# Performance work log

Measured on AMD Instinct MI355X. Metric: run time of the kernel, lower is better.

Reference implementation:

```python
import jax, jax.numpy as jnp
import numpy as np

EPS = 1e-5
DECAY = 0.9        # membrane potential decay
SLOPE = 0.01       # leaky_relu negative slope
HEBB_LR = 0.01     # Hebbian plasticity learning rate
WD = 1e-3          # synapse weight decay
W_CLAMP = 1.0      # synapse weight clamp


def _ln(x, g, b):
    mu = jnp.mean(x, axis=-1, keepdims=True)
    var = jnp.mean((x - mu) ** 2, axis=-1, keepdims=True)
    return (x - mu) * jax.lax.rsqrt(var + EPS) * g + b


def setup_inputs() -> dict:
    key = jax.random.key(0)
    ks = jax.random.split(key, 4)
    B, N = 16384, 1024
    scale = 1.0 / np.sqrt(N)
    return {
        "inputs": jax.random.normal(ks[0], (B, N), dtype=jnp.float32),
        "contribution": jax.random.uniform(ks[1], (B,), dtype=jnp.float32),
        "prev_potential": jnp.zeros((B, N), dtype=jnp.float32),
        "syn_weights": jax.random.normal(ks[2], (N, N), dtype=jnp.float32) * scale,
        "gate_W": jax.random.normal(ks[3], (N, N), dtype=jnp.float32) * scale,
        "gate_b": jnp.zeros((N,), dtype=jnp.float32),
        "pre_gamma": jnp.ones((N,), dtype=jnp.float32),
        "pre_beta": jnp.zeros((N,), dtype=jnp.float32),
        "ln_gamma": jnp.ones((N,), dtype=jnp.float32),
        "ln_beta": jnp.zeros((N,), dtype=jnp.float32),
    }


def reference(inputs, contribution, prev_potential, syn_weights, gate_W, gate_b,
              pre_gamma, pre_beta, ln_gamma, ln_beta):
    B = inputs.shape[0]
    # pre-norm
    x_norm = _ln(inputs, pre_gamma, pre_beta)
    # neuron: recurrent drive through synapse weights + leaky membrane
    pre = x_norm @ syn_weights                      # [B, N]
    potential = DECAY * prev_potential + pre        # new neuron state
    activation = jnp.where(potential >= 0, potential, SLOPE * potential)
    # Hebbian synapse update modulated by per-sample contribution
    hebb = jnp.einsum('bi,bj->ij', activation * contribution[:, None], activation) / B
    new_syn_weights = jnp.clip(syn_weights * (1.0 - WD) + HEBB_LR * hebb,
                               -W_CLAMP, W_CLAMP)
    # gated residual (gate computed on raw inputs)
    gate = jax.nn.sigmoid(inputs @ gate_W.T + gate_b)
    residual = gate * activation + (1.0 - gate) * inputs
    # post-norm (dropout is identity in eval/reference)
    output = _ln(residual, ln_gamma, ln_beta)
    return (output, potential, new_syn_weights)
```

## Files before the change

### kernel.cpp

```cpp
#include <hip/hip_runtime.h>
#include <cstdint>
#include <cstddef>

#define EPS 1e-5f
#define DECAY 0.9f
#define SLOPE 0.01f
#define HEBB_LR 0.01f
#define WDK 1e-3f

typedef float f32x4 __attribute__((ext_vector_type(4)));
typedef __bf16 bf16x8 __attribute__((ext_vector_type(8)));
typedef unsigned short u16;
typedef unsigned int u32;

union U128 { uint4 u; bf16x8 b; };
union Pack16 { u16 s[16]; uint4 q[2]; };
union Pack8  { u16 s[8];  uint4 q; };
union Pack4  { u16 s[4];  uint2 q; };

__device__ __forceinline__ u16 f2b(float f) {
  u32 u = __builtin_bit_cast(u32, f);
  u = u + 0x7FFFu + ((u >> 16) & 1u);
  return (u16)(u >> 16);
}
__device__ __forceinline__ float b2f(u16 h) {
  u32 u = ((u32)h) << 16;
  return __builtin_bit_cast(float, u);
}
__device__ __forceinline__ float wred(float x) {
#pragma unroll
  for (int o = 32; o > 0; o >>= 1) x += __shfl_down(x, o, 64);
  return x;
}

__device__ __forceinline__ void gld16(const u16* g, u16* lds) {
  __builtin_amdgcn_global_load_lds(
      (__attribute__((address_space(1))) void*)g,
      (__attribute__((address_space(3))) void*)lds, 16, 0, 0);
}

__global__ __launch_bounds__(256) void prep_rows(
    const float* __restrict__ in, const float* __restrict__ pg,
    const float* __restrict__ pb, u16* __restrict__ xnb,
    u16* __restrict__ inb, int N) {
  const int row = blockIdx.x, t = threadIdx.x;
  const float* rp = in + (size_t)row * N;
  float4 v = reinterpret_cast<const float4*>(rp)[t];
  float s = v.x + v.y + v.z + v.w;
  float s2 = v.x * v.x + v.y * v.y + v.z * v.z + v.w * v.w;
  s = wred(s); s2 = wred(s2);
  __shared__ float rs_[4], rs2_[4];
  if ((t & 63) == 0) { rs_[t >> 6] = s; rs2_[t >> 6] = s2; }
  __syncthreads();
  float S = rs_[0] + rs_[1] + rs_[2] + rs_[3];
  float S2 = rs2_[0] + rs2_[1] + rs2_[2] + rs2_[3];
  float mu = S / N;
  float var = S2 / N - mu * mu;
  float rstd = rsqrtf(var + EPS);
  float4 g = reinterpret_cast<const float4*>(pg)[t];
  float4 b = reinterpret_cast<const float4*>(pb)[t];
  float xv[4] = {v.x, v.y, v.z, v.w};
  float gv[4] = {g.x, g.y, g.z, g.w};
  float bv[4] = {b.x, b.y, b.z, b.w};
  Pack4 px, pi;
#pragma unroll
  for (int j = 0; j < 4; ++j) {
    px.s[j] = f2b((xv[j] - mu) * rstd * gv[j] + bv[j]);
    pi.s[j] = f2b(xv[j]);
  }
  reinterpret_cast<uint2*>(xnb + (size_t)row * N)[t] = px.q;
  reinterpret_cast<uint2*>(inb + (size_t)row * N)[t] = pi.q;
}

__global__ __launch_bounds__(256) void wconv(const float* __restrict__ W,
                                             u16* __restrict__ Wb, int total) {
  int idx = blockIdx.x * 256 + threadIdx.x;
  size_t off = (size_t)idx * 8;
  if (off >= (size_t)total) return;
  float4 a = *reinterpret_cast<const float4*>(W + off);
  float4 b = *reinterpret_cast<const float4*>(W + off + 4);
  Pack8 p;
  p.s[0] = f2b(a.x); p.s[1] = f2b(a.y); p.s[2] = f2b(a.z); p.s[3] = f2b(a.w);
  p.s[4] = f2b(b.x); p.s[5] = f2b(b.y); p.s[6] = f2b(b.z); p.s[7] = f2b(b.w);
  *reinterpret_cast<uint4*>(Wb + off) = p.q;
}

__global__ __launch_bounds__(256) void wconv_T(const float* __restrict__ W,
                                               u16* __restrict__ Wt, int R, int C) {
  __shared__ float tile[64][65];
  int c0 = blockIdx.x * 64, r0 = blockIdx.y * 64;
  int tr = threadIdx.x >> 2, tc = threadIdx.x & 3;
#pragma unroll
  for (int cc = 0; cc < 4; ++cc) {
    float4 v = *reinterpret_cast<const float4*>(W + (size_t)(r0 + tr) * C + c0 + tc * 16 + cc * 4);
    tile[tr][tc * 16 + cc * 4 + 0] = v.x;
    tile[tr][tc * 16 + cc * 4 + 1] = v.y;
    tile[tr][tc * 16 + cc * 4 + 2] = v.z;
    tile[tr][tc * 16 + cc * 4 + 3] = v.w;
  }
  __syncthreads();
  Pack16 p;
#pragma unroll
  for (int j = 0; j < 16; ++j) p.s[j] = f2b(tile[tc * 16 + j][tr]);
  uint4* dst = reinterpret_cast<uint4*>(Wt + (size_t)(c0 + tr) * R + r0 + tc * 16);
  dst[0] = p.q[0]; dst[1] = p.q[1];
}

__global__ __launch_bounds__(256) void transpose_act(
    const float* __restrict__ pot, const float* __restrict__ contrib,
    u16* __restrict__ actT, u16* __restrict__ actcT, int Brows, int N) {
  __shared__ float tile[64][65];
  __shared__ float csh[64];
  int n0 = blockIdx.x * 64, b0 = blockIdx.y * 64;
  int tr = threadIdx.x >> 2, tc = threadIdx.x & 3;
  if (threadIdx.x < 64) csh[threadIdx.x] = contrib[b0 + threadIdx.x];
#pragma unroll
  for (int cc = 0; cc < 4; ++cc) {
    float4 v = *reinterpret_cast<const float4*>(pot + (size_t)(b0 + tr) * N + n0 + tc * 16 + cc * 4);
    float a0 = v.x >= 0.f ? v.x : SLOPE * v.x;
    float a1 = v.y >= 0.f ? v.y : SLOPE * v.y;
    float a2 = v.z >= 0.f ? v.z : SLOPE * v.z;
    float a3 = v.w >= 0.f ? v.w : SLOPE * v.w;
    tile[tr][tc * 16 + cc * 4 + 0] = a0;
    tile[tr][tc * 16 + cc * 4 + 1] = a1;
    tile[tr][tc * 16 + cc * 4 + 2] = a2;
    tile[tr][tc * 16 + cc * 4 + 3] = a3;
  }
  __syncthreads();
  Pack16 pa, pc;
#pragma unroll
  for (int j = 0; j < 16; ++j) {
    float a = tile[tc * 16 + j][tr];
    pa.s[j] = f2b(a);
    pc.s[j] = f2b(a * csh[tc * 16 + j]);
  }
  size_t obase = (size_t)(n0 + tr) * Brows + b0 + tc * 16;
  uint4* d1 = reinterpret_cast<uint4*>(actT + obase);
  d1[0] = pa.q[0]; d1[1] = pa.q[1];
  uint4* d2 = reinterpret_cast<uint4*>(actcT + obase);
  d2[0] = pc.q[0]; d2[1] = pc.q[1];
}

__global__ __launch_bounds__(256) void fuse_out(
    const float* __restrict__ pot, const u16* __restrict__ gate,
    const u16* __restrict__ inb, const float* __restrict__ lg,
    const float* __restrict__ lb, float* __restrict__ out, int N) {
  const int row = blockIdx.x, t = threadIdx.x;
  size_t base = (size_t)row * N;
  float4 p = reinterpret_cast<const float4*>(pot + base)[t];
  Pack4 xq; xq.q = reinterpret_cast<const uint2*>(inb + base)[t];
  Pack4 gq; gq.q = reinterpret_cast<const uint2*>(gate + base)[t];
  float pv[4] = {p.x, p.y, p.z, p.w};
  float res[4];
  float s = 0.f, s2 = 0.f;
#pragma unroll
  for (int j = 0; j < 4; ++j) {
    float a = pv[j] >= 0.f ? pv[j] : SLOPE * pv[j];
    float gv = b2f(gq.s[j]);
    float xv = b2f(xq.s[j]);
    float r = gv * a + (1.f - gv) * xv;
    res[j] = r; s += r; s2 += r * r;
  }
  s = wred(s); s2 = wred(s2);
  __shared__ float rs_[4], rs2_[4];
  if ((t & 63) == 0) { rs_[t >> 6] = s; rs2_[t >> 6] = s2; }
  __syncthreads();
  float S = rs_[0] + rs_[1] + rs_[2] + rs_[3];
  float S2 = rs2_[0] + rs2_[1] + rs2_[2] + rs2_[3];
  float mu = S / N, var = S2 / N - mu * mu, rstd = rsqrtf(var + EPS);
  float4 g4 = reinterpret_cast<const float4*>(lg)[t];
  float4 b4 = reinterpret_cast<const float4*>(lb)[t];
  float gv[4] = {g4.x, g4.y, g4.z, g4.w}, bv[4] = {b4.x, b4.y, b4.z, b4.w};
  float4 o;
  o.x = (res[0] - mu) * rstd * gv[0] + bv[0];
  o.y = (res[1] - mu) * rstd * gv[1] + bv[1];
  o.z = (res[2] - mu) * rstd * gv[2] + bv[2];
  o.w = (res[3] - mu) * rstd * gv[3] + bv[3];
  reinterpret_cast<float4*>(out + base)[t] = o;
}

template <int EPI>
__global__ __launch_bounds__(512, 2) void gemm2p(
    const u16* __restrict__ A, const u16* __restrict__ Bt,
    int lda, int NT, int Ncols,
    const float* __restrict__ aux,
    float* __restrict__ outF, u16* __restrict__ outB,
    int nbx, int nbxShift, int nbyX) {
  __shared__ __align__(128) char lds[131072];
  const int tid = threadIdx.x;
  const int w = tid >> 6, l = tid & 63;
  const int wr = w >> 2, wc = w & 3;
  const int r16 = l & 15, gq = l >> 4;

  int bx, by, kb;
  if (EPI == 2) {
    bx = blockIdx.x; by = blockIdx.y; kb = blockIdx.z * NT * 64;
  } else {
    int bid = blockIdx.x;
    int xcd = bid & 7, i = bid >> 3;
    by = xcd * nbyX + (i >> nbxShift);
    bx = i & (nbx - 1);
    kb = 0;
  }
  const int m0 = by * 256, n0 = bx * 256;

  const u16* gA[4]; const u16* gB[4]; int dOff[4];
#pragma unroll
  for (int i = 0; i < 4; ++i) {
    int c = i * 512 + tid;
    int row = c >> 3;
    int kg = (c & 7) ^ (row & 7);
    gA[i] = A + (size_t)(m0 + row) * (size_t)lda + kb + kg * 8;
    gB[i] = Bt + (size_t)(n0 + row) * (size_t)lda + kb + kg * 8;
    dOff[i] = c * 16;
  }

  int pA[8], pB[4], kgx[2];
#pragma unroll
  for (int mf = 0; mf < 8; ++mf) pA[mf] = (wr * 128 + mf * 16 + r16) * 128;
#pragma unroll
  for (int nf = 0; nf < 4; ++nf) pB[nf] = (wc * 64 + nf * 16 + r16) * 128;
  kgx[0] = ((gq) ^ (r16 & 7)) * 16;
  kgx[1] = ((4 + gq) ^ (r16 & 7)) * 16;

  f32x4 acc[8][4] = {};

#define STAGE_(t, bufb) { const int _kk = (t) * 64;                           \
  _Pragma("unroll") for (int i = 0; i < 4; ++i)                               \
    gld16(gA[i] + _kk, (u16*)(lds + (bufb) + dOff[i]));                       \
  _Pragma("unroll") for (int i = 0; i < 4; ++i)                               \
    gld16(gB[i] + _kk, (u16*)(lds + (bufb) + 32768 + dOff[i])); }

  STAGE_(0, 0);
  __syncthreads();

  int buf = 0;
  for (int t = 0; t < NT; ++t) {
    if (t + 1 < NT) STAGE_(t + 1, (buf ^ 1) * 65536);
    const char* Ab = lds + buf * 65536;
    const char* Bb = Ab + 32768;
#pragma unroll
    for (int ks = 0; ks < 2; ++ks) {
      U128 af[8], bf[4];
#pragma unroll
      for (int mf = 0; mf < 8; ++mf)
        af[mf].u = *reinterpret_cast<const uint4*>(Ab + pA[mf] + kgx[ks]);
#pragma unroll
      for (int nf = 0; nf < 4; ++nf)
        bf[nf].u = *reinterpret_cast<const uint4*>(Bb + pB[nf] + kgx[ks]);
      __builtin_amdgcn_s_setprio(1);
#pragma unroll
      for (int mf = 0; mf < 8; ++mf)
#pragma unroll
        for (int nf = 0; nf < 4; ++nf)
          acc[mf][nf] = __builtin_amdgcn_mfma_f32_16x16x32_bf16(
              af[mf].b, bf[nf].b, acc[mf][nf], 0, 0, 0);
      __builtin_amdgcn_s_setprio(0);
    }
    __syncthreads();
    buf ^= 1;
  }
#undef STAGE_

  const size_t splitOff =
      (EPI == 2) ? (size_t)blockIdx.z * (size_t)Ncols * (size_t)(gridDim.y * 256) : 0;
#pragma unroll
  for (int mf = 0; mf < 8; ++mf) {
#pragma unroll
    for (int r = 0; r < 4; ++r) {
      const int m = m0 + wr * 128 + mf * 16 + gq * 4 + r;
#pragma unroll
      for (int nf = 0; nf < 4; ++nf) {
        const int n = n0 + wc * 64 + nf * 16 + r16;
        float v = acc[mf][nf][r];
        if (EPI == 0) {
          size_t off = (size_t)m * Ncols + n;
          outF[off] = DECAY * aux[off] + v;
        } else if (EPI == 1) {
          float gl = v + aux[n];
          outB[(size_t)m * Ncols + n] = f2b(1.f / (1.f + __expf(-gl)));
        } else {
          outB[splitOff + (size_t)m * Ncols + n] = f2b(v);
        }
      }
    }
  }
}

__global__ __launch_bounds__(256) void syn_update(
    const float* __restrict__ syn, const u16* __restrict__ part,
    float* __restrict__ outS, int total8, float hebbScale, int nsplit, int NN) {
  int idx = blockIdx.x * 256 + threadIdx.x;
  if (idx >= total8) return;
  float h[8] = {0.f, 0.f, 0.f, 0.f, 0.f, 0.f, 0.f, 0.f};
  for (int sp = 0; sp < nsplit; ++sp) {
    Pack8 p;
    p.q = reinterpret_cast<const uint4*>(part + (size_t)sp * NN)[idx];
#pragma unroll
    for (int j = 0; j < 8; ++j) h[j] += b2f(p.s[j]);
  }
  float4 s0 = reinterpret_cast<const float4*>(syn)[idx * 2];
  float4 s1 = reinterpret_cast<const float4*>(syn)[idx * 2 + 1];
  float sv[8] = {s0.x, s0.y, s0.z, s0.w, s1.x, s1.y, s1.z, s1.w};
  float ov[8];
#pragma unroll
  for (int j = 0; j < 8; ++j)
    ov[j] = fminf(1.f, fmaxf(-1.f, sv[j] * (1.f - WDK) + hebbScale * h[j]));
  float4 o0 = {ov[0], ov[1], ov[2], ov[3]};
  float4 o1 = {ov[4], ov[5], ov[6], ov[7]};
  reinterpret_cast<float4*>(outS)[idx * 2] = o0;
  reinterpret_cast<float4*>(outS)[idx * 2 + 1] = o1;
}

extern "C" void kernel_launch(void* const* d_in, const int* in_sizes, int n_in,
                              void* d_out, int out_size, void* d_ws, size_t ws_size,
                              hipStream_t stream) {
  const float* inputs        = (const float*)d_in[0];
  const float* contribution  = (const float*)d_in[1];
  const float* prev_potential= (const float*)d_in[2];
  const float* syn_weights   = (const float*)d_in[3];
  const float* gate_W        = (const float*)d_in[4];
  const float* gate_b        = (const float*)d_in[5];
  const float* pre_gamma     = (const float*)d_in[6];
  const float* pre_beta      = (const float*)d_in[7];
  const float* ln_gamma      = (const float*)d_in[8];
  const float* ln_beta       = (const float*)d_in[9];

  const int B = in_sizes[1];
  const int N = in_sizes[5];
  const size_t BN = (size_t)B * N;

  float* out_output = (float*)d_out;
  float* out_pot    = out_output + BN;
  float* out_syn    = out_output + 2 * BN;

  char* ws = (char*)d_ws;
  u16* xnb   = (u16*)ws;
  u16* inb   = (u16*)(ws + BN * 2);
  u16* synT  = (u16*)(ws + BN * 4);
  u16* gwb   = (u16*)(ws + BN * 4 + (size_t)N * N * 2);
  u16* gateb = (u16*)(ws + BN * 4 + (size_t)N * N * 4);
  u16* actT  = xnb;
  u16* actcT = inb;
  u16* part  = gateb;

  const int NS = 16;
  const int NT = N / 64;

  prep_rows<<<B, 256, 0, stream>>>(inputs, pre_gamma, pre_beta, xnb, inb, N);
  wconv_T<<<dim3(N / 64, N / 64), 256, 0, stream>>>(syn_weights, synT, N, N);
  wconv<<<(N * N / 8 + 255) / 256, 256, 0, stream>>>(gate_W, gwb, N * N);

  const int nbx = N / 256, nbxShift = 2, nbyX = (B / 256) / 8;
  gemm2p<0><<<(B / 256) * (N / 256), 512, 0, stream>>>(
      xnb, synT, N, NT, N, prev_potential, out_pot, nullptr, nbx, nbxShift, nbyX);
  gemm2p<1><<<(B / 256) * (N / 256), 512, 0, stream>>>(
      inb, gwb, N, NT, N, gate_b, nullptr, gateb, nbx, nbxShift, nbyX);
  fuse_out<<<B, 256, 0, stream>>>(out_pot, gateb, inb, ln_gamma, ln_beta, out_output, N);
  transpose_act<<<dim3(N / 64, B / 64), 256, 0, stream>>>(
      out_pot, contribution, actT, actcT, B, N);
  gemm2p<2><<<dim3(N / 256, N / 256, NS), 512, 0, stream>>>(
      actcT, actT, B, (B / NS) / 64, N, nullptr, nullptr, part, 0, 0, 0);
  syn_update<<<(N * N / 8 + 255) / 256, 256, 0, stream>>>(
      syn_weights, part, out_syn, N * N / 8, HEBB_LR / (float)B, NS, N * N);
}
```

Measured before the change: 438.0 us.

## Replace 256x256 GEMM tiles with 128x256 tiles, 4 waves, K-step 32

Rewrites the shared GEMM kernel to use 128x256 output tiles computed by 256 threads (4 waves of 64x128), with a K-step of 32 and a smaller 48KB double-buffered LDS footprint. It also changes the swizzle to suit 64-byte rows, and flattens the split-K Hebbian GEMM grid with XCD-aware z mapping. The aim is more resident blocks per CU and better load balance and cache locality across XCDs. In exchange, arithmetic intensity per tile drops, and the loop runs twice as many iterations, each with a barrier.

```diff
diff --git a/kernel.cpp b/kernel.cpp
--- a/kernel.cpp
+++ b/kernel.cpp
@@ -33,7 +33,7 @@
   return x;
 }
 
-__device__ __forceinline__ void gld16(const u16* g, u16* lds) {
+__device__ __forceinline__ void gld16(const u16* g, const char* lds) {
   __builtin_amdgcn_global_load_lds(
       (__attribute__((address_space(1))) void*)g,
       (__attribute__((address_space(3))) void*)lds, 16, 0, 0);
@@ -180,98 +180,102 @@
 }
 
 template <int EPI>
-__global__ __launch_bounds__(512, 2) void gemm2p(
+__global__ __launch_bounds__(256, 2) void gemm_w2(
     const u16* __restrict__ A, const u16* __restrict__ Bt,
     int lda, int NT, int Ncols,
     const float* __restrict__ aux,
     float* __restrict__ outF, u16* __restrict__ outB,
-    int nbx, int nbxShift, int nbyX) {
-  __shared__ __align__(128) char lds[131072];
+    int nbyX, int zPerXcd, int zRows) {
+  __shared__ __align__(128) char lds[49152];
   const int tid = threadIdx.x;
   const int w = tid >> 6, l = tid & 63;
-  const int wr = w >> 2, wc = w & 3;
+  const int wr = w >> 1, wc = w & 1;
   const int r16 = l & 15, gq = l >> 4;
 
-  int bx, by, kb;
-  if (EPI == 2) {
-    bx = blockIdx.x; by = blockIdx.y; kb = blockIdx.z * NT * 64;
-  } else {
-    int bid = blockIdx.x;
-    int xcd = bid & 7, i = bid >> 3;
-    by = xcd * nbyX + (i >> nbxShift);
-    bx = i & (nbx - 1);
-    kb = 0;
-  }
-  const int m0 = by * 256, n0 = bx * 256;
-
-  const u16* gA[4]; const u16* gB[4]; int dOff[4];
-#pragma unroll
-  for (int i = 0; i < 4; ++i) {
-    int c = i * 512 + tid;
-    int row = c >> 3;
-    int kg = (c & 7) ^ (row & 7);
-    gA[i] = A + (size_t)(m0 + row) * (size_t)lda + kb + kg * 8;
-    gB[i] = Bt + (size_t)(n0 + row) * (size_t)lda + kb + kg * 8;
-    dOff[i] = c * 16;
-  }
-
-  int pA[8], pB[4], kgx[2];
-#pragma unroll
-  for (int mf = 0; mf < 8; ++mf) pA[mf] = (wr * 128 + mf * 16 + r16) * 128;
-#pragma unroll
-  for (int nf = 0; nf < 4; ++nf) pB[nf] = (wc * 64 + nf * 16 + r16) * 128;
-  kgx[0] = ((gq) ^ (r16 & 7)) * 16;
-  kgx[1] = ((4 + gq) ^ (r16 & 7)) * 16;
-
-  f32x4 acc[8][4] = {};
-
-#define STAGE_(t, bufb) { const int _kk = (t) * 64;                           \
-  _Pragma("unroll") for (int i = 0; i < 4; ++i)                               \
-    gld16(gA[i] + _kk, (u16*)(lds + (bufb) + dOff[i]));                       \
-  _Pragma("unroll") for (int i = 0; i < 4; ++i)                               \
-    gld16(gB[i] + _kk, (u16*)(lds + (bufb) + 32768 + dOff[i])); }
+  int bx, by, z, kb;
+  {
+    const int xcd = blockIdx.x & 7, i = blockIdx.x >> 3;
+    bx = i & 3;
+    if (EPI == 2) {
+      const int j = i >> 2;
+      by = j & 7;
+      z = xcd * zPerXcd + (j >> 3);
+      kb = z * (NT * 32);
+    } else {
+      by = xcd * nbyX + (i >> 2);
+      z = 0; kb = 0;
+    }
+  }
+  const int m0 = by * 128, n0 = bx * 256;
+
+  const u16* gA[2]; const u16* gB[4]; int dA[2], dB[4];
+#pragma unroll
+  for (int j = 0; j < 2; ++j) {
+    int c = j * 256 + tid, row = c >> 2;
+    int kg = (c & 3) ^ ((row >> 1) & 3);
+    gA[j] = A + (size_t)(m0 + row) * (size_t)lda + kb + kg * 8;
+    dA[j] = c * 16;
+  }
+#pragma unroll
+  for (int j = 0; j < 4; ++j) {
+    int c = j * 256 + tid, row = c >> 2;
+    int kg = (c & 3) ^ ((row >> 1) & 3);
+    gB[j] = Bt + (size_t)(n0 + row) * (size_t)lda + kb + kg * 8;
+    dB[j] = 8192 + c * 16;
+  }
+
+  const int kgx = (gq ^ ((r16 >> 1) & 3)) * 16;
+  int pA[4], pB[8];
+#pragma unroll
+  for (int mf = 0; mf < 4; ++mf) pA[mf] = (wr * 64 + mf * 16 + r16) * 64 + kgx;
+#pragma unroll
+  for (int nf = 0; nf < 8; ++nf) pB[nf] = 8192 + (wc * 128 + nf * 16 + r16) * 64 + kgx;
+
+  f32x4 acc[4][8] = {};
+
+#define STAGE_(t, bufb) { const int _kk = (t) * 32;                           \
+  _Pragma("unroll") for (int j = 0; j < 2; ++j)                               \
+    gld16(gA[j] + _kk, lds + (bufb) + dA[j]);                                 \
+  _Pragma("unroll") for (int j = 0; j < 4; ++j)                               \
+    gld16(gB[j] + _kk, lds + (bufb) + dB[j]); }
 
   STAGE_(0, 0);
   __syncthreads();
 
   int buf = 0;
   for (int t = 0; t < NT; ++t) {
-    if (t + 1 < NT) STAGE_(t + 1, (buf ^ 1) * 65536);
-    const char* Ab = lds + buf * 65536;
-    const char* Bb = Ab + 32768;
-#pragma unroll
-    for (int ks = 0; ks < 2; ++ks) {
-      U128 af[8], bf[4];
-#pragma unroll
-      for (int mf = 0; mf < 8; ++mf)
-        af[mf].u = *reinterpret_cast<const uint4*>(Ab + pA[mf] + kgx[ks]);
-#pragma unroll
-      for (int nf = 0; nf < 4; ++nf)
-        bf[nf].u = *reinterpret_cast<const uint4*>(Bb + pB[nf] + kgx[ks]);
-      __builtin_amdgcn_s_setprio(1);
-#pragma unroll
-      for (int mf = 0; mf < 8; ++mf)
-#pragma unroll
-        for (int nf = 0; nf < 4; ++nf)
-          acc[mf][nf] = __builtin_amdgcn_mfma_f32_16x16x32_bf16(
-              af[mf].b, bf[nf].b, acc[mf][nf], 0, 0, 0);
-      __builtin_amdgcn_s_setprio(0);
-    }
+    if (t + 1 < NT) STAGE_(t + 1, (buf ^ 1) * 24576);
+    const char* bb = lds + buf * 24576;
+    U128 af[4], bf[8];
+#pragma unroll
+    for (int mf = 0; mf < 4; ++mf)
+      af[mf].u = *reinterpret_cast<const uint4*>(bb + pA[mf]);
+#pragma unroll
+    for (int nf = 0; nf < 8; ++nf)
+      bf[nf].u = *reinterpret_cast<const uint4*>(bb + pB[nf]);
+    __builtin_amdgcn_s_setprio(1);
+#pragma unroll
+    for (int mf = 0; mf < 4; ++mf)
+#pragma unroll
+      for (int nf = 0; nf < 8; ++nf)
+        acc[mf][nf] = __builtin_amdgcn_mfma_f32_16x16x32_bf16(
+            af[mf].b, bf[nf].b, acc[mf][nf], 0, 0, 0);
+    __builtin_amdgcn_s_setprio(0);
     __syncthreads();
     buf ^= 1;
   }
 #undef STAGE_
 
   const size_t splitOff =
-      (EPI == 2) ? (size_t)blockIdx.z * (size_t)Ncols * (size_t)(gridDim.y * 256) : 0;
-#pragma unroll
-  for (int mf = 0; mf < 8; ++mf) {
+      (EPI == 2) ? (size_t)z * (size_t)Ncols * (size_t)zRows : 0;
+#pragma unroll
+  for (int mf = 0; mf < 4; ++mf) {
 #pragma unroll
     for (int r = 0; r < 4; ++r) {
-      const int m = m0 + wr * 128 + mf * 16 + gq * 4 + r;
-#pragma unroll
-      for (int nf = 0; nf < 4; ++nf) {
-        const int n = n0 + wc * 64 + nf * 16 + r16;
+      const int m = m0 + wr * 64 + mf * 16 + gq * 4 + r;
+#pragma unroll
+      for (int nf = 0; nf < 8; ++nf) {
+        const int n = n0 + wc * 128 + nf * 16 + r16;
         float v = acc[mf][nf][r];
         if (EPI == 0) {
           size_t off = (size_t)m * Ncols + n;
@@ -345,22 +349,22 @@
   u16* part  = gateb;
 
   const int NS = 16;
-  const int NT = N / 64;
+  const int NT = N / 32;
 
   prep_rows<<<B, 256, 0, stream>>>(inputs, pre_gamma, pre_beta, xnb, inb, N);
   wconv_T<<<dim3(N / 64, N / 64), 256, 0, stream>>>(syn_weights, synT, N, N);
   wconv<<<(N * N / 8 + 255) / 256, 256, 0, stream>>>(gate_W, gwb, N * N);
 
-  const int nbx = N / 256, nbxShift = 2, nbyX = (B / 256) / 8;
-  gemm2p<0><<<(B / 256) * (N / 256), 512, 0, stream>>>(
-      xnb, synT, N, NT, N, prev_potential, out_pot, nullptr, nbx, nbxShift, nbyX);
-  gemm2p<1><<<(B / 256) * (N / 256), 512, 0, stream>>>(
-      inb, gwb, N, NT, N, gate_b, nullptr, gateb, nbx, nbxShift, nbyX);
+  const int nbyX = (B / 128) / 8;
+  gemm_w2<0><<<(B / 128) * (N / 256), 256, 0, stream>>>(
+      xnb, synT, N, NT, N, prev_potential, out_pot, nullptr, nbyX, 0, 0);
+  gemm_w2<1><<<(B / 128) * (N / 256), 256, 0, stream>>>(
+      inb, gwb, N, NT, N, gate_b, nullptr, gateb, nbyX, 0, 0);
   fuse_out<<<B, 256, 0, stream>>>(out_pot, gateb, inb, ln_gamma, ln_beta, out_output, N);
   transpose_act<<<dim3(N / 64, B / 64), 256, 0, stream>>>(
       out_pot, contribution, actT, actcT, B, N);
-  gemm2p<2><<<dim3(N / 256, N / 256, NS), 512, 0, stream>>>(
-      actcT, actT, B, (B / NS) / 64, N, nullptr, nullptr, part, 0, 0, 0);
+  gemm_w2<2><<<(N / 128) * (N / 256) * NS, 256, 0, stream>>>(
+      actcT, actT, B, (B / NS) / 32, N, nullptr, nullptr, part, 0, NS / 8, N);
   syn_update<<<(N * N / 8 + 255) / 256, 256, 0, stream>>>(
       syn_weights, part, out_syn, N * N / 8, HEBB_LR / (float)B, NS, N * N);
 }
```

New measurement: 430.2 us. Within noise of the previous version (-1.8%).
